# Performance work log

Measured on AMD Instinct MI355X. Metric: run time of the kernel, lower is better.

The kernel has to match this reference:

```python
import jax, jax.numpy as jnp
import numpy as np

EPS = 1e-5


def _bn_relu(h, gamma, beta):
    # BatchNorm1d in training mode: stats over all but the last (channel) dim
    m = h.reshape(-1, h.shape[-1])
    mu = jnp.mean(m, axis=0)
    var = jnp.var(m, axis=0)
    return jax.nn.relu((h - mu) * jax.lax.rsqrt(var + EPS) * gamma + beta)


def setup_inputs() -> dict:
    key = jax.random.key(0)
    ks = jax.random.split(key, 16)
    B, N, D, OUT = 64, 64, 64, 128
    T = 2 * D          # object_tuple_size = 128
    HG, HF = 256, 128  # hidden_dim_g, hidden_dim_f

    def lin(k, i, o):
        return (jax.random.normal(k, (i, o), jnp.float32) / np.sqrt(i).astype(np.float32),
                jnp.zeros((o,), jnp.float32))

    inp = {"x": jax.random.normal(ks[0], (B, N, D), jnp.float32)}
    # G: depth-3 Linear-BN-ReLU, dims T -> HG -> HG -> T
    for i, (a, b) in enumerate([(T, HG), (HG, HG), (HG, T)]):
        W, bb = lin(ks[1 + i], a, b)
        inp[f"gW{i}"] = W
        inp[f"gb{i}"] = bb
        inp[f"gg{i}"] = jnp.ones((b,), jnp.float32)
        inp[f"gB{i}"] = jnp.zeros((b,), jnp.float32)
    # F: depth-2 Linear-BN-ReLU, dims T -> HF -> T, then Linear(T, OUT)
    for i, (a, b) in enumerate([(T, HF), (HF, T)]):
        W, bb = lin(ks[5 + i], a, b)
        inp[f"fW{i}"] = W
        inp[f"fb{i}"] = bb
        inp[f"fg{i}"] = jnp.ones((b,), jnp.float32)
        inp[f"fB{i}"] = jnp.zeros((b,), jnp.float32)
    inp["foW"], inp["fob"] = lin(ks[8], T, OUT)
    return inp


def reference(x, gW0, gb0, gg0, gB0, gW1, gb1, gg1, gB1, gW2, gb2, gg2, gB2,
              fW0, fb0, fg0, fB0, fW1, fb1, fg1, fB1, foW, fob):
    B, N, D = x.shape
    # GroupObjectsIntoPairs: all ordered pairs -> (B, N*N, 2D)
    xi = jnp.broadcast_to(x[:, :, None, :], (B, N, N, D))
    xj = jnp.broadcast_to(x[:, None, :, :], (B, N, N, D))
    h = jnp.concatenate([xi, xj], axis=-1).reshape(B, N * N, 2 * D)
    # G: per-pair MLP
    for W, b, g, be in ((gW0, gb0, gg0, gB0), (gW1, gb1, gg1, gB1), (gW2, gb2, gg2, gB2)):
        h = _bn_relu(h @ W + b, g, be)
    # sum over pair dimension (no layer norm)
    s = h.sum(axis=1)  # (B, 2D)
    # F: MLP + final linear
    for W, b, g, be in ((fW0, fb0, fg0, fB0), (fW1, fb1, fg1, fB1)):
        s = _bn_relu(s @ W + b, g, be)
    return s @ foW + fob  # (B, OUT)
```

## Files before the change

kernel.cpp:

```cpp
#include <hip/hip_runtime.h>


typedef _Float16 half8 __attribute__((ext_vector_type(8)));
typedef _Float16 half4_t __attribute__((ext_vector_type(4)));
typedef float float4_t __attribute__((ext_vector_type(4)));

static constexpr float kEps = 1e-5f;
static constexpr float kM = 262144.f;

static constexpr size_t OFF_U   = 0;
static constexpr size_t OFF_V   = OFF_U  + (size_t)4096*256*4;
static constexpr size_t OFF_UP  = OFF_V  + (size_t)4096*256*4;
static constexpr size_t OFF_VP  = OFF_UP + (size_t)4096*256*2;
static constexpr size_t OFF_W1T = OFF_VP + (size_t)4096*256*2;
static constexpr size_t OFF_W2T = OFF_W1T + (size_t)256*256*2;
static constexpr size_t OFF_Z1  = OFF_W2T + (size_t)128*256*2;
static constexpr size_t OFF_ST0 = OFF_Z1 + (size_t)262144*256*2;
static constexpr size_t OFF_C0S = OFF_ST0 + (size_t)64*4*256*4;
static constexpr size_t OFF_C0T = OFF_C0S + 1024;
static constexpr size_t OFF_C1S = OFF_C0T + 1024;
static constexpr size_t OFF_C1T = OFF_C1S + 1024;
static constexpr size_t OFF_C2S = OFF_C1T + 1024;
static constexpr size_t OFF_C2T = OFF_C2S + 512;
static constexpr size_t OFF_ST1 = OFF_C2T + 512;
static constexpr size_t OFF_ST2 = OFF_ST1 + (size_t)32*512*4;
static constexpr size_t OFF_SB  = OFF_ST2 + (size_t)32*256*4;
static constexpr size_t OFF_FST0 = OFF_SB + (size_t)64*128*4;
static constexpr size_t OFF_FST1 = OFF_FST0 + 1024;
static constexpr size_t ZERO_BYTES = (size_t)32*512*4 + (size_t)32*256*4
                                   + (size_t)64*128*4 + 2048;
static constexpr size_t OFF_FZ0  = OFF_FST1 + 1024;
static constexpr size_t OFF_FZ1  = OFF_FZ0 + (size_t)64*128*4;
static constexpr size_t OFF_CF0S = OFF_FZ1 + (size_t)64*128*4;
static constexpr size_t OFF_CF0T = OFF_CF0S + 512;
static constexpr size_t OFF_CF1S = OFF_CF0T + 512;
static constexpr size_t OFF_CF1T = OFF_CF1S + 512;

static __device__ inline half8 relu8(half8 s) {
#pragma unroll
  for (int e = 0; e < 8; ++e) s[e] = s[e] > (_Float16)0 ? s[e] : (_Float16)0;
  return s;
}

__global__ __launch_bounds__(256) void k_wt(const float* __restrict__ gW1,
                                            const float* __restrict__ gW2,
                                            _Float16* __restrict__ W1T,
                                            _Float16* __restrict__ W2T) {
  int idx = blockIdx.x * 256 + threadIdx.x;
  if (idx < 65536) {
    int n = idx >> 8, k = idx & 255;
    W1T[idx] = (_Float16)gW1[k * 256 + n];
  } else if (idx < 98304) {
    int j = idx - 65536;
    int n = j >> 8, k = j & 255;
    W2T[j] = (_Float16)gW2[k * 128 + n];
  }
}

__global__ __launch_bounds__(256) void k_prep(const float* __restrict__ x,
                                              const float* __restrict__ gW0,
                                              float* __restrict__ U,
                                              float* __restrict__ V) {
  __shared__ __align__(16) float sX[32 * 64];
  int t = threadIdx.x;
  int p0 = blockIdx.x * 32;
  int by = blockIdx.y;
  int hsel = by >> 1;
  int cbase = (by & 1) * 128;
#pragma unroll
  for (int it = 0; it < 2; ++it) {
    int f4 = (it * 256 + t) * 4;
    *(float4_t*)(sX + f4) = *(const float4_t*)(x + (size_t)p0 * 64 + f4);
  }
  __syncthreads();
  int r = t >> 3, cg = (t & 7) * 16;
  const float* Wb = gW0 + (size_t)(hsel * 64) * 256 + cbase + cg;
  float acc[16];
#pragma unroll
  for (int j = 0; j < 16; ++j) acc[j] = 0.f;
  for (int k = 0; k < 64; ++k) {
    float xv = sX[r * 64 + k];
    const float4_t* wr = (const float4_t*)(Wb + (size_t)k * 256);
    float4_t w0 = wr[0], w1 = wr[1], w2 = wr[2], w3 = wr[3];
#pragma unroll
    for (int j = 0; j < 4; ++j) {
      acc[j]      += xv * w0[j];
      acc[4 + j]  += xv * w1[j];
      acc[8 + j]  += xv * w2[j];
      acc[12 + j] += xv * w3[j];
    }
  }
  float* outp = (hsel ? V : U) + (size_t)(p0 + r) * 256 + cbase + cg;
#pragma unroll
  for (int q = 0; q < 4; ++q) {
    float4_t o = {acc[q * 4], acc[q * 4 + 1], acc[q * 4 + 2], acc[q * 4 + 3]};
    *(float4_t*)(outp + q * 4) = o;
  }
}

__global__ __launch_bounds__(256) void k_stats0(const float* __restrict__ U,
                                                const float* __restrict__ V,
                                                float* __restrict__ st0) {
  int b = blockIdx.x, c = threadIdx.x;
  float su = 0, su2 = 0, sv = 0, sv2 = 0;
  for (int i = 0; i < 64; ++i) {
    float u = U[(size_t)(b * 64 + i) * 256 + c];
    float v = V[(size_t)(b * 64 + i) * 256 + c];
    su += u; su2 += u * u; sv += v; sv2 += v * v;
  }
  st0[(b * 4 + 0) * 256 + c] = su;
  st0[(b * 4 + 1) * 256 + c] = su2;
  st0[(b * 4 + 2) * 256 + c] = sv;
  st0[(b * 4 + 3) * 256 + c] = sv2;
}

__global__ __launch_bounds__(256) void k_bn0(const float* __restrict__ st0,
                                             const float* __restrict__ gb0,
                                             const float* __restrict__ gg0,
                                             const float* __restrict__ gB0,
                                             float* __restrict__ c0s,
                                             float* __restrict__ c0t) {
  int c = threadIdx.x;
  float su = 0, su2 = 0, sv = 0, sv2 = 0, cross = 0;
  for (int b = 0; b < 64; ++b) {
    float a  = st0[(b * 4 + 0) * 256 + c];
    float a2 = st0[(b * 4 + 1) * 256 + c];
    float v  = st0[(b * 4 + 2) * 256 + c];
    float v2 = st0[(b * 4 + 3) * 256 + c];
    su += a; su2 += a2; sv += v; sv2 += v2; cross += a * v;
  }
  float b0 = gb0[c];
  float sumz  = 64.f * (su + sv) + kM * b0;
  float sumzz = 64.f * (su2 + sv2) + 2.f * cross + 2.f * b0 * 64.f * (su + sv) + kM * b0 * b0;
  float mu = sumz / kM;
  float var = sumzz / kM - mu * mu;
  float sc = gg0[c] * rsqrtf(var + kEps);
  c0s[c] = sc;
  c0t[c] = gB0[c] + sc * (b0 - mu);
}

__global__ __launch_bounds__(256) void k_uv(const float* __restrict__ U,
                                            const float* __restrict__ V,
                                            const float* __restrict__ c0s,
                                            const float* __restrict__ c0t,
                                            _Float16* __restrict__ Up,
                                            _Float16* __restrict__ Vp) {
  int idx = blockIdx.x * 256 + threadIdx.x;
  int e4 = idx * 4;
  int c4 = e4 & 255;
  float4_t u = *(const float4_t*)(U + e4);
  float4_t v = *(const float4_t*)(V + e4);
  float4_t s = *(const float4_t*)(c0s + c4);
  float4_t tt = *(const float4_t*)(c0t + c4);
  half4_t hu, hv;
#pragma unroll
  for (int e = 0; e < 4; ++e) {
    hu[e] = (_Float16)(u[e] * s[e] + tt[e]);
    hv[e] = (_Float16)(v[e] * s[e]);
  }
  *(half4_t*)(Up + e4) = hu;
  *(half4_t*)(Vp + e4) = hv;
}

__global__ __launch_bounds__(256) void k_gemm1(const _Float16* __restrict__ Up,
                                               const _Float16* __restrict__ Vp,
                                               const _Float16* __restrict__ W1T,
                                               const float* __restrict__ gb1,
                                               _Float16* __restrict__ Z1,
                                               float* __restrict__ stats1) {
  __shared__ __align__(16) _Float16 sU[2 * 264];
  __shared__ __align__(16) _Float16 sV[64 * 264];
  __shared__ __align__(16) _Float16 sW[128 * 72];
  const int t = threadIdx.x;
  const int bx = blockIdx.x;
  const int n0 = blockIdx.y * 128;
  const int b = bx >> 5;
  const int i0 = (bx & 31) * 2;
  const long R0 = (long)bx * 128;

  if (t < 64) {
    int row = t >> 5, k8 = (t & 31) * 8;
    *(half8*)(sU + row * 264 + k8) =
        *(const half8*)(Up + (size_t)(b * 64 + i0 + row) * 256 + k8);
  }
#pragma unroll
  for (int it = 0; it < 8; ++it) {
    int flat = it * 256 + t;
    int row = flat >> 5, k8 = (flat & 31) * 8;
    *(half8*)(sV + row * 264 + k8) =
        *(const half8*)(Vp + (size_t)(b * 64 + row) * 256 + k8);
  }

  const int wid = t >> 6, L = t & 63;
  const int wrow = wid >> 1, wcol = wid & 1;
  const int quad = L >> 4, l15 = L & 15;

  float4_t acc[4][4];
#pragma unroll
  for (int mt = 0; mt < 4; ++mt)
#pragma unroll
    for (int nt = 0; nt < 4; ++nt) acc[mt][nt] = (float4_t){0.f, 0.f, 0.f, 0.f};

  for (int kc = 0; kc < 4; ++kc) {
    __syncthreads();
#pragma unroll
    for (int it = 0; it < 4; ++it) {
      int flat = it * 256 + t;
      int n = flat >> 3, k8 = (flat & 7) * 8;
      *(half8*)(sW + n * 72 + k8) =
          *(const half8*)(W1T + (size_t)(n0 + n) * 256 + kc * 64 + k8);
    }
    __syncthreads();
#pragma unroll
    for (int ks = 0; ks < 2; ++ks) {
      const int kk = ks * 32 + quad * 8;
      const int kg = kc * 64 + kk;
      const half8 u = *(const half8*)(sU + wrow * 264 + kg);
      half8 afr[4];
#pragma unroll
      for (int mt = 0; mt < 4; ++mt) {
        half8 v = *(const half8*)(sV + (mt * 16 + l15) * 264 + kg);
        afr[mt] = relu8(u + v);
      }
      half8 bfr[4];
#pragma unroll
      for (int nt = 0; nt < 4; ++nt)
        bfr[nt] = *(const half8*)(sW + (wcol * 64 + nt * 16 + l15) * 72 + kk);
#pragma unroll
      for (int mt = 0; mt < 4; ++mt)
#pragma unroll
        for (int nt = 0; nt < 4; ++nt)
          acc[mt][nt] = __builtin_amdgcn_mfma_f32_16x16x32_f16(afr[mt], bfr[nt],
                                                               acc[mt][nt], 0, 0, 0);
    }
  }

  const int rep = bx & 31;
#pragma unroll
  for (int nt = 0; nt < 4; ++nt) {
    const int col = n0 + wcol * 64 + nt * 16 + l15;
    const float b1c = gb1[col];
    float sz = 0.f, szz = 0.f;
#pragma unroll
    for (int mt = 0; mt < 4; ++mt) {
      const size_t rowb = (size_t)(R0 + wrow * 64 + mt * 16 + quad * 4);
#pragma unroll
      for (int r = 0; r < 4; ++r) {
        float z = acc[mt][nt][r] + b1c;
        Z1[(rowb + r) * 256 + col] = (_Float16)z;
        sz += z;
        szz += z * z;
      }
    }
    sz += __shfl_xor(sz, 16, 64);
    sz += __shfl_xor(sz, 32, 64);
    szz += __shfl_xor(szz, 16, 64);
    szz += __shfl_xor(szz, 32, 64);
    if (quad == 0) {
      atomicAdd(stats1 + rep * 512 + col, sz);
      atomicAdd(stats1 + rep * 512 + 256 + col, szz);
    }
  }
}

__global__ __launch_bounds__(256) void k_bn1(const float* __restrict__ stats1,
                                             const float* __restrict__ gg1,
                                             const float* __restrict__ gB1,
                                             float* __restrict__ c1s,
                                             float* __restrict__ c1t) {
  int c = threadIdx.x;
  float S = 0.f, S2 = 0.f;
  for (int rp = 0; rp < 32; ++rp) {
    S += stats1[rp * 512 + c];
    S2 += stats1[rp * 512 + 256 + c];
  }
  float mu = S / kM;
  float var = S2 / kM - mu * mu;
  float sc = gg1[c] * rsqrtf(var + kEps);
  c1s[c] = sc;
  c1t[c] = gB1[c] - sc * mu;
}

template <int FINAL>
__global__ __launch_bounds__(256) void k_gemm23(const _Float16* __restrict__ Z1,
                                                const _Float16* __restrict__ W2T,
                                                const float* __restrict__ c1s,
                                                const float* __restrict__ c1t,
                                                const float* __restrict__ gb2,
                                                const float* __restrict__ c2s,
                                                const float* __restrict__ c2t,
                                                float* __restrict__ stats2,
                                                float* __restrict__ sbuf) {
  __shared__ __align__(16) _Float16 sA[128 * 72];
  __shared__ __align__(16) _Float16 sW[128 * 72];
  __shared__ __align__(16) float sS[256];
  __shared__ __align__(16) float sT[256];
  const int t = threadIdx.x;
  const int bx = blockIdx.x;
  const long R0 = (long)bx * 128;
  sS[t] = c1s[t];
  sT[t] = c1t[t];

  const int wid = t >> 6, L = t & 63;
  const int wrow = wid >> 1, wcol = wid & 1;
  const int quad = L >> 4, l15 = L & 15;

  float4_t acc[4][4];
#pragma unroll
  for (int mt = 0; mt < 4; ++mt)
#pragma unroll
    for (int nt = 0; nt < 4; ++nt) acc[mt][nt] = (float4_t){0.f, 0.f, 0.f, 0.f};

  for (int kc = 0; kc < 4; ++kc) {
    __syncthreads();
#pragma unroll
    for (int it = 0; it < 4; ++it) {
      int flat = it * 256 + t;
      int row = flat >> 3, k8 = (flat & 7) * 8;
      int kg = kc * 64 + k8;
      half8 hv = *(const half8*)(Z1 + ((size_t)R0 + row) * 256 + kg);
      float4_t s0 = *(const float4_t*)(sS + kg);
      float4_t s1 = *(const float4_t*)(sS + kg + 4);
      float4_t t0 = *(const float4_t*)(sT + kg);
      float4_t t1 = *(const float4_t*)(sT + kg + 4);
      half8 ov;
#pragma unroll
      for (int e = 0; e < 4; ++e) {
        ov[e]     = (_Float16)fmaxf(s0[e] * (float)hv[e] + t0[e], 0.f);
        ov[4 + e] = (_Float16)fmaxf(s1[e] * (float)hv[4 + e] + t1[e], 0.f);
      }
      *(half8*)(sA + row * 72 + k8) = ov;
    }
#pragma unroll
    for (int it = 0; it < 4; ++it) {
      int flat = it * 256 + t;
      int n = flat >> 3, k8 = (flat & 7) * 8;
      *(half8*)(sW + n * 72 + k8) =
          *(const half8*)(W2T + (size_t)n * 256 + kc * 64 + k8);
    }
    __syncthreads();
#pragma unroll
    for (int ks = 0; ks < 2; ++ks) {
      const int kk = ks * 32 + quad * 8;
      half8 afr[4];
#pragma unroll
      for (int mt = 0; mt < 4; ++mt)
        afr[mt] = *(const half8*)(sA + (wrow * 64 + mt * 16 + l15) * 72 + kk);
      half8 bfr[4];
#pragma unroll
      for (int nt = 0; nt < 4; ++nt)
        bfr[nt] = *(const half8*)(sW + (wcol * 64 + nt * 16 + l15) * 72 + kk);
#pragma unroll
      for (int mt = 0; mt < 4; ++mt)
#pragma unroll
        for (int nt = 0; nt < 4; ++nt)
          acc[mt][nt] = __builtin_amdgcn_mfma_f32_16x16x32_f16(afr[mt], bfr[nt],
                                                               acc[mt][nt], 0, 0, 0);
    }
  }

  const int rep = bx & 31;
#pragma unroll
  for (int nt = 0; nt < 4; ++nt) {
    const int col = wcol * 64 + nt * 16 + l15;
    const float b2c = gb2[col];
    if (FINAL) {
      const float s2 = c2s[col], t2 = c2t[col];
      float ps = 0.f;
#pragma unroll
      for (int mt = 0; mt < 4; ++mt)
#pragma unroll
        for (int r = 0; r < 4; ++r)
          ps += fmaxf(s2 * (acc[mt][nt][r] + b2c) + t2, 0.f);
      ps += __shfl_xor(ps, 16, 64);
      ps += __shfl_xor(ps, 32, 64);
      if (quad == 0) atomicAdd(sbuf + (bx >> 5) * 128 + col, ps);
    } else {
      float sz = 0.f, szz = 0.f;
#pragma unroll
      for (int mt = 0; mt < 4; ++mt)
#pragma unroll
        for (int r = 0; r < 4; ++r) {
          float z = acc[mt][nt][r] + b2c;
          sz += z;
          szz += z * z;
        }
      sz += __shfl_xor(sz, 16, 64);
      sz += __shfl_xor(sz, 32, 64);
      szz += __shfl_xor(szz, 16, 64);
      szz += __shfl_xor(szz, 32, 64);
      if (quad == 0) {
        atomicAdd(stats2 + rep * 256 + col, sz);
        atomicAdd(stats2 + rep * 256 + 128 + col, szz);
      }
    }
  }
}

__global__ __launch_bounds__(128) void k_bn2(const float* __restrict__ stats2,
                                             const float* __restrict__ gg2,
                                             const float* __restrict__ gB2,
                                             float* __restrict__ c2s,
                                             float* __restrict__ c2t) {
  int c = threadIdx.x;
  float S = 0.f, S2 = 0.f;
  for (int rp = 0; rp < 32; ++rp) {
    S += stats2[rp * 256 + c];
    S2 += stats2[rp * 256 + 128 + c];
  }
  float mu = S / kM;
  float var = S2 / kM - mu * mu;
  float sc = gg2[c] * rsqrtf(var + kEps);
  c2s[c] = sc;
  c2t[c] = gB2[c] - sc * mu;
}

template <bool APPLY_BN, bool STATS>
__global__ __launch_bounds__(256) void k_fg(const float* __restrict__ in,
                                            const float* __restrict__ cs,
                                            const float* __restrict__ ct,
                                            const float* __restrict__ W,
                                            const float* __restrict__ bias,
                                            float* __restrict__ zout,
                                            float* __restrict__ stats) {
  __shared__ __align__(16) float sIn[8 * 128];
  __shared__ __align__(16) float sZ[8 * 128];
  const int t = threadIdx.x;
  const int r0 = blockIdx.x * 8;
  {
    int flat = t * 4;
    int col = flat & 127;
    float4_t v = *(const float4_t*)(in + (size_t)r0 * 128 + flat);
    if (APPLY_BN) {
      float4_t s = *(const float4_t*)(cs + col);
      float4_t sh = *(const float4_t*)(ct + col);
#pragma unroll
      for (int e = 0; e < 4; ++e) v[e] = fmaxf(s[e] * v[e] + sh[e], 0.f);
    }
    *(float4_t*)(sIn + flat) = v;
  }
  __syncthreads();

  const int r = t >> 5;
  const int c4 = (t & 31) * 4;
  float4_t acc = *(const float4_t*)(bias + c4);
  for (int k = 0; k < 128; ++k) {
    float xv = sIn[r * 128 + k];
    float4_t w = *(const float4_t*)(W + (size_t)k * 128 + c4);
#pragma unroll
    for (int e = 0; e < 4; ++e) acc[e] += xv * w[e];
  }
  *(float4_t*)(zout + (size_t)(r0 + r) * 128 + c4) = acc;

  if (STATS) {
    *(float4_t*)(sZ + r * 128 + c4) = acc;
    __syncthreads();
    if (t < 128) {
      float S = 0.f, S2 = 0.f;
#pragma unroll
      for (int rr = 0; rr < 8; ++rr) {
        float z = sZ[rr * 128 + t];
        S += z;
        S2 += z * z;
      }
      atomicAdd(stats + t, S);
      atomicAdd(stats + 128 + t, S2);
    }
  }
}

__global__ __launch_bounds__(128) void k_fbn(const float* __restrict__ stats,
                                             const float* __restrict__ g,
                                             const float* __restrict__ B,
                                             float* __restrict__ cs,
                                             float* __restrict__ ct) {
  int c = threadIdx.x;
  float S = stats[c], S2 = stats[128 + c];
  float mu = S / 64.f;
  float var = S2 / 64.f - mu * mu;
  float sc = g[c] * rsqrtf(var + kEps);
  cs[c] = sc;
  ct[c] = B[c] - sc * mu;
}

extern "C" void kernel_launch(void* const* d_in, const int* in_sizes, int n_in,
                              void* d_out, int out_size, void* d_ws, size_t ws_size,
                              hipStream_t stream) {
  (void)in_sizes; (void)n_in; (void)out_size; (void)ws_size;
  const float* x   = (const float*)d_in[0];
  const float* gW0 = (const float*)d_in[1];
  const float* gb0 = (const float*)d_in[2];
  const float* gg0 = (const float*)d_in[3];
  const float* gB0 = (const float*)d_in[4];
  const float* gW1 = (const float*)d_in[5];
  const float* gb1 = (const float*)d_in[6];
  const float* gg1 = (const float*)d_in[7];
  const float* gB1 = (const float*)d_in[8];
  const float* gW2 = (const float*)d_in[9];
  const float* gb2 = (const float*)d_in[10];
  const float* gg2 = (const float*)d_in[11];
  const float* gB2 = (const float*)d_in[12];
  const float* fW0 = (const float*)d_in[13];
  const float* fb0 = (const float*)d_in[14];
  const float* fg0 = (const float*)d_in[15];
  const float* fB0 = (const float*)d_in[16];
  const float* fW1 = (const float*)d_in[17];
  const float* fb1 = (const float*)d_in[18];
  const float* fg1 = (const float*)d_in[19];
  const float* fB1 = (const float*)d_in[20];
  const float* foW = (const float*)d_in[21];
  const float* fob = (const float*)d_in[22];
  float* out = (float*)d_out;

  char* ws = (char*)d_ws;
  float*    U    = (float*)(ws + OFF_U);
  float*    V    = (float*)(ws + OFF_V);
  _Float16* Up   = (_Float16*)(ws + OFF_UP);
  _Float16* Vp   = (_Float16*)(ws + OFF_VP);
  _Float16* W1T  = (_Float16*)(ws + OFF_W1T);
  _Float16* W2T  = (_Float16*)(ws + OFF_W2T);
  _Float16* Z1   = (_Float16*)(ws + OFF_Z1);
  float*    st0  = (float*)(ws + OFF_ST0);
  float*    c0s  = (float*)(ws + OFF_C0S);
  float*    c0t  = (float*)(ws + OFF_C0T);
  float*    c1s  = (float*)(ws + OFF_C1S);
  float*    c1t  = (float*)(ws + OFF_C1T);
  float*    c2s  = (float*)(ws + OFF_C2S);
  float*    c2t  = (float*)(ws + OFF_C2T);
  float*    st1  = (float*)(ws + OFF_ST1);
  float*    st2  = (float*)(ws + OFF_ST2);
  float*    sbuf = (float*)(ws + OFF_SB);
  float*    fst0 = (float*)(ws + OFF_FST0);
  float*    fst1 = (float*)(ws + OFF_FST1);
  float*    fz0  = (float*)(ws + OFF_FZ0);
  float*    fz1  = (float*)(ws + OFF_FZ1);
  float*    cf0s = (float*)(ws + OFF_CF0S);
  float*    cf0t = (float*)(ws + OFF_CF0T);
  float*    cf1s = (float*)(ws + OFF_CF1S);
  float*    cf1t = (float*)(ws + OFF_CF1T);

  hipMemsetAsync(ws + OFF_ST1, 0, ZERO_BYTES, stream);

  k_wt<<<384, 256, 0, stream>>>(gW1, gW2, W1T, W2T);
  k_prep<<<dim3(128, 4), 256, 0, stream>>>(x, gW0, U, V);
  k_stats0<<<64, 256, 0, stream>>>(U, V, st0);
  k_bn0<<<1, 256, 0, stream>>>(st0, gb0, gg0, gB0, c0s, c0t);
  k_uv<<<1024, 256, 0, stream>>>(U, V, c0s, c0t, Up, Vp);
  k_gemm1<<<dim3(2048, 2), 256, 0, stream>>>(Up, Vp, W1T, gb1, Z1, st1);
  k_bn1<<<1, 256, 0, stream>>>(st1, gg1, gB1, c1s, c1t);
  k_gemm23<0><<<2048, 256, 0, stream>>>(Z1, W2T, c1s, c1t, gb2, c2s, c2t, st2, sbuf);
  k_bn2<<<1, 128, 0, stream>>>(st2, gg2, gB2, c2s, c2t);
  k_gemm23<1><<<2048, 256, 0, stream>>>(Z1, W2T, c1s, c1t, gb2, c2s, c2t, st2, sbuf);
  k_fg<false, true><<<8, 256, 0, stream>>>(sbuf, nullptr, nullptr, fW0, fb0, fz0, fst0);
  k_fbn<<<1, 128, 0, stream>>>(fst0, fg0, fB0, cf0s, cf0t);
  k_fg<true, true><<<8, 256, 0, stream>>>(fz0, cf0s, cf0t, fW1, fb1, fz1, fst1);
  k_fbn<<<1, 128, 0, stream>>>(fst1, fg1, fB1, cf1s, cf1t);
  k_fg<true, false><<<8, 256, 0, stream>>>(fz1, cf1s, cf1t, foW, fob, out, nullptr);
}
```

Measured before the change: 339.3 us.

## Materialize layer-3 pre-activations in fp16 instead of recomputing GEMM for reduction

Replaces the two-pass recompute of the third G-layer GEMM with a single GEMM that stores fp16 Z2 and its statistics, followed by a lightweight BN+ReLU+sum reduction kernel over Z2. BN1 scale/shift is also applied in packed fp16 arithmetic when loading A tiles. This trades a second full GEMM pass over Z1 for writing and rereading a 64 MB fp16 Z2 buffer, and adds fp16 rounding in the BN1 affine and in Z2. The new path runs only when the workspace is large enough, otherwise it falls back to the old path.

```diff
diff --git a/kernel.cpp b/kernel.cpp
--- a/kernel.cpp
+++ b/kernel.cpp
@@ -35,6 +35,9 @@
 static constexpr size_t OFF_CF0T = OFF_CF0S + 512;
 static constexpr size_t OFF_CF1S = OFF_CF0T + 512;
 static constexpr size_t OFF_CF1T = OFF_CF1S + 512;
+static constexpr size_t OFF_C1H  = OFF_CF1T + 512;
+static constexpr size_t OFF_Z2   = OFF_C1H + 1024;
+static constexpr size_t WS_REQUIRED = OFF_Z2 + (size_t)262144*128*2;
 
 static __device__ inline half8 relu8(half8 s) {
 #pragma unroll
@@ -267,7 +270,8 @@
                                              const float* __restrict__ gg1,
                                              const float* __restrict__ gB1,
                                              float* __restrict__ c1s,
-                                             float* __restrict__ c1t) {
+                                             float* __restrict__ c1t,
+                                             _Float16* __restrict__ c1h) {
   int c = threadIdx.x;
   float S = 0.f, S2 = 0.f;
   for (int rp = 0; rp < 32; ++rp) {
@@ -277,8 +281,107 @@
   float mu = S / kM;
   float var = S2 / kM - mu * mu;
   float sc = gg1[c] * rsqrtf(var + kEps);
+  float sh = gB1[c] - sc * mu;
   c1s[c] = sc;
-  c1t[c] = gB1[c] - sc * mu;
+  c1t[c] = sh;
+  c1h[c] = (_Float16)sc;
+  c1h[256 + c] = (_Float16)sh;
+}
+
+__global__ __launch_bounds__(256) void k_gemm2(const _Float16* __restrict__ Z1,
+                                               const _Float16* __restrict__ W2T,
+                                               const _Float16* __restrict__ c1h,
+                                               const float* __restrict__ gb2,
+                                               _Float16* __restrict__ Z2,
+                                               float* __restrict__ stats2) {
+  __shared__ __align__(16) _Float16 sA[128 * 72];
+  __shared__ __align__(16) _Float16 sW[128 * 72];
+  __shared__ __align__(16) _Float16 sSh[256];
+  __shared__ __align__(16) _Float16 sTh[256];
+  const int t = threadIdx.x;
+  const int bx = blockIdx.x;
+  const long R0 = (long)bx * 128;
+  sSh[t] = c1h[t];
+  sTh[t] = c1h[256 + t];
+
+  const int wid = t >> 6, L = t & 63;
+  const int wrow = wid >> 1, wcol = wid & 1;
+  const int quad = L >> 4, l15 = L & 15;
+
+  float4_t acc[4][4];
+#pragma unroll
+  for (int mt = 0; mt < 4; ++mt)
+#pragma unroll
+    for (int nt = 0; nt < 4; ++nt) acc[mt][nt] = (float4_t){0.f, 0.f, 0.f, 0.f};
+
+  for (int kc = 0; kc < 4; ++kc) {
+    __syncthreads();
+#pragma unroll
+    for (int it = 0; it < 4; ++it) {
+      int flat = it * 256 + t;
+      int row = flat >> 3, k8 = (flat & 7) * 8;
+      int kg = kc * 64 + k8;
+      half8 hv = *(const half8*)(Z1 + ((size_t)R0 + row) * 256 + kg);
+      half8 hs = *(const half8*)(sSh + kg);
+      half8 ht = *(const half8*)(sTh + kg);
+      half8 ov = hv * hs + ht;
+      ov = relu8(ov);
+      *(half8*)(sA + row * 72 + k8) = ov;
+    }
+#pragma unroll
+    for (int it = 0; it < 4; ++it) {
+      int flat = it * 256 + t;
+      int n = flat >> 3, k8 = (flat & 7) * 8;
+      *(half8*)(sW + n * 72 + k8) =
+          *(const half8*)(W2T + (size_t)n * 256 + kc * 64 + k8);
+    }
+    __syncthreads();
+#pragma unroll
+    for (int ks = 0; ks < 2; ++ks) {
+      const int kk = ks * 32 + quad * 8;
+      half8 afr[4];
+#pragma unroll
+      for (int mt = 0; mt < 4; ++mt)
+        afr[mt] = *(const half8*)(sA + (wrow * 64 + mt * 16 + l15) * 72 + kk);
+      half8 bfr[4];
+#pragma unroll
+      for (int nt = 0; nt < 4; ++nt)
+        bfr[nt] = *(const half8*)(sW + (wcol * 64 + nt * 16 + l15) * 72 + kk);
+#pragma unroll
+      for (int mt = 0; mt < 4; ++mt)
+#pragma unroll
+        for (int nt = 0; nt < 4; ++nt)
+          acc[mt][nt] = __builtin_amdgcn_mfma_f32_16x16x32_f16(afr[mt], bfr[nt],
+                                                               acc[mt][nt], 0, 0, 0);
+    }
+  }
+
+  const int rep = bx & 31;
+#pragma unroll
+  for (int nt = 0; nt < 4; ++nt) {
+    const int col = wcol * 64 + nt * 16 + l15;
+    const float b2c = gb2[col];
+    float sz = 0.f, szz = 0.f;
+#pragma unroll
+    for (int mt = 0; mt < 4; ++mt) {
+      const size_t rowb = (size_t)(R0 + wrow * 64 + mt * 16 + quad * 4);
+#pragma unroll
+      for (int r = 0; r < 4; ++r) {
+        float z = acc[mt][nt][r] + b2c;
+        Z2[(rowb + r) * 128 + col] = (_Float16)z;
+        sz += z;
+        szz += z * z;
+      }
+    }
+    sz += __shfl_xor(sz, 16, 64);
+    sz += __shfl_xor(sz, 32, 64);
+    szz += __shfl_xor(szz, 16, 64);
+    szz += __shfl_xor(szz, 32, 64);
+    if (quad == 0) {
+      atomicAdd(stats2 + rep * 256 + col, sz);
+      atomicAdd(stats2 + rep * 256 + 128 + col, szz);
+    }
+  }
 }
 
 template <int FINAL>
@@ -415,6 +518,49 @@
   c2t[c] = gB2[c] - sc * mu;
 }
 
+__global__ __launch_bounds__(256) void k_red(const _Float16* __restrict__ Z2,
+                                             const float* __restrict__ c2s,
+                                             const float* __restrict__ c2t,
+                                             float* __restrict__ sbuf) {
+  __shared__ float sR[256 * 8];
+  const int t = threadIdx.x;
+  const int bx = blockIdx.x;
+  const int b = bx >> 5;
+  const long row0 = (long)bx * 128;
+  const int rr = t >> 4;
+  const int c8 = (t & 15) * 8;
+
+  float4_t s0 = *(const float4_t*)(c2s + c8);
+  float4_t s1 = *(const float4_t*)(c2s + c8 + 4);
+  float4_t t0 = *(const float4_t*)(c2t + c8);
+  float4_t t1 = *(const float4_t*)(c2t + c8 + 4);
+
+  float acc[8];
+#pragma unroll
+  for (int e = 0; e < 8; ++e) acc[e] = 0.f;
+#pragma unroll
+  for (int it = 0; it < 8; ++it) {
+    long row = row0 + it * 16 + rr;
+    half8 h = *(const half8*)(Z2 + row * 128 + c8);
+#pragma unroll
+    for (int e = 0; e < 4; ++e) {
+      acc[e]     += fmaxf(s0[e] * (float)h[e] + t0[e], 0.f);
+      acc[4 + e] += fmaxf(s1[e] * (float)h[4 + e] + t1[e], 0.f);
+    }
+  }
+#pragma unroll
+  for (int e = 0; e < 8; ++e) sR[t * 8 + e] = acc[e];
+  __syncthreads();
+  if (t < 128) {
+    int g = t >> 3, e = t & 7;
+    float S = 0.f;
+#pragma unroll
+    for (int rr2 = 0; rr2 < 16; ++rr2) S += sR[rr2 * 128 + t];
+    (void)g; (void)e;
+    atomicAdd(sbuf + b * 128 + t, S);
+  }
+}
+
 template <bool APPLY_BN, bool STATS>
 __global__ __launch_bounds__(256) void k_fg(const float* __restrict__ in,
                                             const float* __restrict__ cs,
@@ -486,7 +632,7 @@
 extern "C" void kernel_launch(void* const* d_in, const int* in_sizes, int n_in,
                               void* d_out, int out_size, void* d_ws, size_t ws_size,
                               hipStream_t stream) {
-  (void)in_sizes; (void)n_in; (void)out_size; (void)ws_size;
+  (void)in_sizes; (void)n_in; (void)out_size;
   const float* x   = (const float*)d_in[0];
   const float* gW0 = (const float*)d_in[1];
   const float* gb0 = (const float*)d_in[2];
@@ -538,6 +684,8 @@
   float*    cf0t = (float*)(ws + OFF_CF0T);
   float*    cf1s = (float*)(ws + OFF_CF1S);
   float*    cf1t = (float*)(ws + OFF_CF1T);
+  _Float16* c1h  = (_Float16*)(ws + OFF_C1H);
+  _Float16* Z2   = (_Float16*)(ws + OFF_Z2);
 
   hipMemsetAsync(ws + OFF_ST1, 0, ZERO_BYTES, stream);
 
@@ -547,10 +695,18 @@
   k_bn0<<<1, 256, 0, stream>>>(st0, gb0, gg0, gB0, c0s, c0t);
   k_uv<<<1024, 256, 0, stream>>>(U, V, c0s, c0t, Up, Vp);
   k_gemm1<<<dim3(2048, 2), 256, 0, stream>>>(Up, Vp, W1T, gb1, Z1, st1);
-  k_bn1<<<1, 256, 0, stream>>>(st1, gg1, gB1, c1s, c1t);
-  k_gemm23<0><<<2048, 256, 0, stream>>>(Z1, W2T, c1s, c1t, gb2, c2s, c2t, st2, sbuf);
-  k_bn2<<<1, 128, 0, stream>>>(st2, gg2, gB2, c2s, c2t);
-  k_gemm23<1><<<2048, 256, 0, stream>>>(Z1, W2T, c1s, c1t, gb2, c2s, c2t, st2, sbuf);
+  k_bn1<<<1, 256, 0, stream>>>(st1, gg1, gB1, c1s, c1t, c1h);
+
+  if (ws_size >= WS_REQUIRED) {
+    k_gemm2<<<2048, 256, 0, stream>>>(Z1, W2T, c1h, gb2, Z2, st2);
+    k_bn2<<<1, 128, 0, stream>>>(st2, gg2, gB2, c2s, c2t);
+    k_red<<<2048, 256, 0, stream>>>(Z2, c2s, c2t, sbuf);
+  } else {
+    k_gemm23<0><<<2048, 256, 0, stream>>>(Z1, W2T, c1s, c1t, gb2, c2s, c2t, st2, sbuf);
+    k_bn2<<<1, 128, 0, stream>>>(st2, gg2, gB2, c2s, c2t);
+    k_gemm23<1><<<2048, 256, 0, stream>>>(Z1, W2T, c1s, c1t, gb2, c2s, c2t, st2, sbuf);
+  }
+
   k_fg<false, true><<<8, 256, 0, stream>>>(sbuf, nullptr, nullptr, fW0, fb0, fz0, fst0);
   k_fbn<<<1, 128, 0, stream>>>(fst0, fg0, fB0, cf0s, cf0t);
   k_fg<true, true><<<8, 256, 0, stream>>>(fz0, cf0s, cf0t, fW1, fb1, fz1, fst1);
```

Measured after the change: 322.1 us. 5.1% less time.
